# Optimization experiments

Measured on AMD Instinct MI355X. Metric: run time of the kernel, lower is better.

Reference implementation:

```python
import jax, jax.numpy as jnp
import numpy as np
from jax import lax

BN_EPS = 1e-5


def conv3x3(x, w):
    # x: [B,C,H,W], w: [O,I,3,3] -> [B,O,H,W], stride 1, SAME padding, no bias
    return lax.conv_general_dilated(x, w, (1, 1), 'SAME',
                                    dimension_numbers=('NCHW', 'OIHW', 'NCHW'))


def batchnorm_eval(x, gamma, beta, mean, var):
    inv = gamma / jnp.sqrt(var + BN_EPS)
    return x * inv[None, :, None, None] + (beta - mean * inv)[None, :, None, None]


def avg_pool3(x):
    # AvgPool2d(3, stride=1, padding=1) with count_include_pad=True -> sum/9
    s = lax.reduce_window(x, 0.0, lax.add, (1, 1, 3, 3), (1, 1, 1, 1), 'SAME')
    return s / 9.0


def max_pool3(x):
    return lax.reduce_window(x, -jnp.inf, lax.max, (1, 1, 3, 3), (1, 1, 1, 1), 'SAME')


def setup_inputs() -> dict:
    key = jax.random.key(0)
    ks = jax.random.split(key, 20)
    B, C, H, W = 8, 256, 48, 48
    sc = 0.05
    inp = {
        'ftr': jax.random.normal(ks[0], (B, C, H, W), jnp.float32),
        'wq': jax.random.normal(ks[1], (C, C, 1, 1), jnp.float32) * sc,
        'bq': jax.random.normal(ks[2], (C,), jnp.float32) * sc,
        'wk': jax.random.normal(ks[3], (C, C, 1, 1), jnp.float32) * sc,
        'bk': jax.random.normal(ks[4], (C,), jnp.float32) * sc,
        'wv': jax.random.normal(ks[5], (C, C, 1, 1), jnp.float32) * sc,
        'bv': jax.random.normal(ks[6], (C,), jnp.float32) * sc,
        'delta': jnp.array([0.1], jnp.float32),
        'w_rbc': jax.random.normal(ks[7], (C, C, 3, 3), jnp.float32) * sc,
        'g1': jnp.ones((C,), jnp.float32),
        'b1': jnp.zeros((C,), jnp.float32),
        'm1': jnp.zeros((C,), jnp.float32),
        'v1': jnp.ones((C,), jnp.float32),
        'w_rbc2': jax.random.normal(ks[8], (C, 2 * C, 3, 3), jnp.float32) * sc,
        'g2': jnp.ones((C,), jnp.float32),
        'b2': jnp.zeros((C,), jnp.float32),
        'm2': jnp.zeros((C,), jnp.float32),
        'v2': jnp.ones((C,), jnp.float32),
    }
    return inp


def reference(ftr, wq, bq, wk, bk, wv, bv, delta, w_rbc, g1, b1, m1, v1,
              w_rbc2, g2, b2, m2, v2):
    B, C, H, W = ftr.shape
    P = H * W
    x = ftr.reshape(B, C, P)  # [B,C,P]
    # 1x1 convs as channel matmuls
    q = jnp.einsum('oc,bcp->bop', wq[:, :, 0, 0], x) + bq[None, :, None]
    k = jnp.einsum('oc,bcp->bop', wk[:, :, 0, 0], x) + bk[None, :, None]
    v = jnp.einsum('oc,bcp->bop', wv[:, :, 0, 0], x) + bv[None, :, None]
    # scores[b,i,j] = sum_c q[b,c,i] * k[b,c,j]; softmax over i (dim=1)
    scores = jnp.einsum('bci,bcj->bij', q, k)
    weights = jax.nn.softmax(scores, axis=1)
    G = jnp.einsum('bci,bij->bcj', v, weights).reshape(B, C, H, W)
    out = delta[0] * G + ftr
    # conv_rbc: conv3x3 -> BN(eval) -> ReLU, then sigmoid gate
    out = jax.nn.relu(batchnorm_eval(conv3x3(out, w_rbc), g1, b1, m1, v1))
    gate = jax.nn.sigmoid(out)
    ftr_avg = avg_pool3(ftr) * gate
    ftr_max = max_pool3(ftr) * gate
    cat = jnp.concatenate((ftr_max, ftr_avg), axis=1)  # [B,2C,H,W]
    out = jax.nn.relu(batchnorm_eval(conv3x3(cat, w_rbc2), g2, b2, m2, v2))
    return out
```

## Files before the change

### kernel.cpp

```cpp
#include <hip/hip_runtime.h>
#include <math.h>

#define NB   8
#define CCH  256
#define PPX  2304
#define CPb  (CCH*PPX)
#define NTOT (NB*CPb)
#define PSQ  (PPX*PPX)
#define PADIMG 2500

typedef short short8_t __attribute__((ext_vector_type(8)));
typedef float f4_t __attribute__((ext_vector_type(4)));

__device__ __forceinline__ float relu_(float x){ return x > 0.f ? x : 0.f; }

__device__ __forceinline__ unsigned short f2bf(float f) {
  unsigned int u = __builtin_bit_cast(unsigned int, f);
  u += 0x7fffu + ((u >> 16) & 1u);
  return (unsigned short)(u >> 16);
}
__device__ __forceinline__ float bf2f(unsigned short h) {
  unsigned int u = ((unsigned int)h) << 16;
  return __builtin_bit_cast(float, u);
}
__device__ __forceinline__ unsigned int pack2(float a, float b) {
  return (unsigned int)f2bf(a) | ((unsigned int)f2bf(b) << 16);
}

__device__ __forceinline__ void gll16(const void* g, void* l) {
  __builtin_amdgcn_global_load_lds(
      (const __attribute__((address_space(1))) unsigned int*)g,
      (__attribute__((address_space(3))) unsigned int*)l, 16, 0, 0);
}

__global__ __launch_bounds__(256) void castw(
    const float* __restrict__ w, unsigned short* __restrict__ o, int n)
{
  const int i = blockIdx.x * 256 + threadIdx.x;
  if (i < n) o[i] = f2bf(w[i]);
}

__global__ __launch_bounds__(256) void repack_w(
    const float* __restrict__ w, unsigned short* __restrict__ wr, int Cin)
{
  const int idx = blockIdx.x * 256 + threadIdx.x;
  const int total = 9 * 256 * Cin;
  if (idx >= total) return;
  const int c = idx % Cin;
  const int rest = idx / Cin;
  const int o = rest % 256;
  const int tap = rest / 256;
  wr[idx] = f2bf(w[((size_t)o * Cin + c) * 9 + tap]);
}

__global__ __launch_bounds__(256) void transpose_cast(
    const float* __restrict__ ftr, unsigned short* __restrict__ xt)
{
  const int p0 = blockIdx.x * 64, c0 = blockIdx.y * 64, b = blockIdx.z;
  const int t = threadIdx.x;
  __shared__ unsigned short T[64][72];
  #pragma unroll
  for (int pass = 0; pass < 4; pass++) {
    const int cr = pass * 16 + (t >> 4);
    const int pc = (t & 15) * 4;
    float4 v = *(const float4*)&ftr[((size_t)(b * 256 + c0 + cr)) * PPX + p0 + pc];
    T[pc + 0][cr] = f2bf(v.x); T[pc + 1][cr] = f2bf(v.y);
    T[pc + 2][cr] = f2bf(v.z); T[pc + 3][cr] = f2bf(v.w);
  }
  __syncthreads();
  #pragma unroll
  for (int pass = 0; pass < 2; pass++) {
    const int pr = pass * 32 + (t >> 3);
    const int cc = (t & 7) * 8;
    *(uint4*)&xt[((size_t)(b * PPX + p0 + pr)) * 256 + c0 + cc] = *(const uint4*)&T[pr][cc];
  }
}

template<int EPI>
__global__ __launch_bounds__(256) void gemm_nt(
    const unsigned short* __restrict__ A, long Ab,
    const unsigned short* __restrict__ B, long Bb, int K,
    unsigned short* __restrict__ O, long Ob, int ldo,
    const float* __restrict__ bias,
    const float* __restrict__ ftr, const float* __restrict__ delta, int bstart)
{
  const int t = threadIdx.x;
  const int ln = t & 63;
  const int wid = t >> 6;
  const int wm = (wid & 1) * 64, wn = (wid >> 1) * 64;
  const int lm = ln & 15, lg = ln >> 4;
  const int m0 = blockIdx.x * 128, n0 = blockIdx.y * 128;
  const long bz = blockIdx.z;
  const unsigned short* Ap = A + bz * Ab;
  const unsigned short* Bp = B + bz * Bb;

  __shared__ __align__(16) unsigned short As[128 * 32];
  __shared__ __align__(16) unsigned short Bs[128 * 32];

  const int sR = ln >> 2, sP = ln & 3;
  const int fbase = lm * 32 + (((lg + (lm >> 2)) & 3) * 8);

  f4_t acc[4][4];
  #pragma unroll
  for (int i = 0; i < 4; i++)
    #pragma unroll
    for (int j = 0; j < 4; j++) acc[i][j] = (f4_t){0.f, 0.f, 0.f, 0.f};

  for (int k0 = 0; k0 < K; k0 += 32) {
    __syncthreads();
    #pragma unroll
    for (int i = wid; i < 8; i += 4) {
      const int R = i * 16 + sR;
      const int l = (sP - (R >> 2)) & 3;
      gll16(Ap + (size_t)(m0 + R) * K + k0 + l * 8, As + i * 512);
      gll16(Bp + (size_t)(n0 + R) * K + k0 + l * 8, Bs + i * 512);
    }
    __syncthreads();
    short8_t a[4], b[4];
    #pragma unroll
    for (int ti = 0; ti < 4; ti++)
      a[ti] = *(const short8_t*)(As + (wm + ti * 16) * 32 + fbase);
    #pragma unroll
    for (int tj = 0; tj < 4; tj++)
      b[tj] = *(const short8_t*)(Bs + (wn + tj * 16) * 32 + fbase);
    #pragma unroll
    for (int ti = 0; ti < 4; ti++)
      #pragma unroll
      for (int tj = 0; tj < 4; tj++)
        acc[ti][tj] = __builtin_amdgcn_mfma_f32_16x16x32_bf16(
            a[ti], b[tj], acc[ti][tj], 0, 0, 0);
  }

  if (EPI == 3) {
    const int b = bstart + (int)bz;
    const float d0 = delta[0];
    #pragma unroll
    for (int ti = 0; ti < 4; ti++) {
      const int mb = m0 + wm + ti * 16 + (lg << 2);
      #pragma unroll
      for (int tj = 0; tj < 4; tj++) {
        const int n = n0 + wn + tj * 16 + lm;
        const int y = n / 48, x = n - (n / 48) * 48;
        const size_t pp = (size_t)(y + 1) * 50 + (x + 1);
        float vr[4];
        #pragma unroll
        for (int r = 0; r < 4; r++)
          vr[r] = d0 * acc[ti][tj][r] + ftr[((size_t)(b * 256 + mb + r)) * PPX + n];
        uint2 o;
        o.x = pack2(vr[0], vr[1]);
        o.y = pack2(vr[2], vr[3]);
        *(uint2*)(O + ((size_t)b * PADIMG + pp) * 256 + mb) = o;
      }
    }
  } else {
    #pragma unroll
    for (int ti = 0; ti < 4; ti++) {
      const int mb = m0 + wm + ti * 16 + (lg << 2);
      #pragma unroll
      for (int tj = 0; tj < 4; tj++) {
        const int n = n0 + wn + tj * 16 + lm;
        float add0 = 0.f, add1 = 0.f, add2 = 0.f, add3 = 0.f;
        if (EPI == 1) { add0 = bias[mb]; add1 = bias[mb+1]; add2 = bias[mb+2]; add3 = bias[mb+3]; }
        if (EPI == 2) { add0 = add1 = add2 = add3 = bias[n]; }
        uint2 o;
        o.x = pack2(acc[ti][tj][0] + add0, acc[ti][tj][1] + add1);
        o.y = pack2(acc[ti][tj][2] + add2, acc[ti][tj][3] + add3);
        *(uint2*)(O + bz * Ob + (size_t)n * ldo + mb) = o;
      }
    }
  }
}

__global__ __launch_bounds__(256) void rowstats(
    unsigned short* __restrict__ St, long sstride)
{
  const int j = blockIdx.x, bb = blockIdx.y;
  unsigned short* row = St + (long)bb * sstride + (size_t)j * PPX;
  const int t = threadIdx.x;

  float v[16];
  int nv = 0;
  float m = -1e30f;
  for (int ch = t; ch < 288; ch += 256) {
    const uint4 d = *(const uint4*)(row + ch * 8);
    const unsigned int* dp = (const unsigned int*)&d;
    #pragma unroll
    for (int q = 0; q < 4; q++) {
      v[nv]     = bf2f((unsigned short)(dp[q] & 0xffffu));
      v[nv + 1] = bf2f((unsigned short)(dp[q] >> 16));
      m = fmaxf(m, fmaxf(v[nv], v[nv + 1]));
      nv += 2;
    }
  }
  __shared__ float red[256];
  red[t] = m; __syncthreads();
  for (int s = 128; s > 0; s >>= 1) {
    if (t < s) red[t] = fmaxf(red[t], red[t + s]);
    __syncthreads();
  }
  m = red[0]; __syncthreads();
  float sum = 0.f;
  for (int u = 0; u < nv; u++) { v[u] = expf(v[u] - m); sum += v[u]; }
  red[t] = sum; __syncthreads();
  for (int s = 128; s > 0; s >>= 1) {
    if (t < s) red[t] += red[t + s];
    __syncthreads();
  }
  const float inv = 1.f / red[0];
  int u = 0;
  for (int ch = t; ch < 288; ch += 256) {
    unsigned int res[4];
    #pragma unroll
    for (int q = 0; q < 4; q++) {
      res[q] = pack2(v[u] * inv, v[u + 1] * inv);
      u += 2;
    }
    *(uint4*)(row + ch * 8) = *(const uint4*)res;
  }
}

template<bool OUT_BF16>
__global__ __launch_bounds__(128) void conv_mfma(
    const unsigned short* __restrict__ act_p, int Cin,
    const unsigned short* __restrict__ wr,
    const float* __restrict__ gamma, const float* __restrict__ beta,
    const float* __restrict__ mean,  const float* __restrict__ var,
    void* __restrict__ outv)
{
  const int t  = threadIdx.x;
  const int wv = t >> 6;
  const int ln = t & 63;
  const int lm = ln & 15;
  const int lg = ln >> 4;

  const int bx = blockIdx.x;
  const int bb = bx / 18;
  const int p0 = (bx % 18) * 128;
  const int m0 = blockIdx.y * 64;

  __shared__ __align__(16) unsigned short Bs[240 * 32];
  __shared__ __align__(16) unsigned short As[9 * 64 * 32];

  const int qbase = p0 + 2 * (p0 / 48);
  int qoff[4];
  #pragma unroll
  for (int tj = 0; tj < 4; tj++) {
    const int p = p0 + wv * 64 + tj * 16 + lm;
    qoff[tj] = (p - p0) + 2 * (p / 48 - p0 / 48) + 51;
  }

  const int sR = ln >> 2, sP = ln & 3;
  const int abase = lm * 32 + (((lg + (lm >> 2)) & 3) * 8);

  f4_t acc[4][4];
  #pragma unroll
  for (int i = 0; i < 4; i++)
    #pragma unroll
    for (int j = 0; j < 4; j++) acc[i][j] = (f4_t){0.f, 0.f, 0.f, 0.f};

  for (int c0 = 0; c0 < Cin; c0 += 32) {
    __syncthreads();
    const unsigned short* gb = act_p + ((size_t)bb * PADIMG) * Cin + c0;
    for (int i = wv; i < 15; i += 2) {
      const int R = i * 16 + sR;
      int Rg = qbase + R;
      if (Rg > PADIMG - 1) Rg = PADIMG - 1;
      const int l = (sP - (R >> 2)) & 3;
      gll16(gb + (size_t)Rg * Cin + l * 8, Bs + i * 512);
    }
    for (int i = wv; i < 36; i += 2) {
      const int R = i * 16 + sR;
      const int tap = R >> 6, mr = R & 63;
      const int l = (sP - (R >> 2)) & 3;
      gll16(wr + ((size_t)(tap * 256 + m0 + mr)) * Cin + c0 + l * 8, As + i * 512);
    }
    __syncthreads();
    #pragma unroll
    for (int ky = 0; ky < 3; ky++) {
      #pragma unroll
      for (int kx = 0; kx < 3; kx++) {
        const int off = (ky - 1) * 50 + (kx - 1);
        const int tap = ky * 3 + kx;
        short8_t a[4], b[4];
        #pragma unroll
        for (int ti = 0; ti < 4; ti++)
          a[ti] = *(const short8_t*)(As + tap * 2048 + ti * 512 + abase);
        #pragma unroll
        for (int tj = 0; tj < 4; tj++) {
          const int R = qoff[tj] + off;
          const int slot = (lg + (R >> 2)) & 3;
          b[tj] = *(const short8_t*)(Bs + R * 32 + slot * 8);
        }
        #pragma unroll
        for (int ti = 0; ti < 4; ti++)
          #pragma unroll
          for (int tj = 0; tj < 4; tj++)
            acc[ti][tj] = __builtin_amdgcn_mfma_f32_16x16x32_bf16(
                a[ti], b[tj], acc[ti][tj], 0, 0, 0);
      }
    }
  }

  #pragma unroll
  for (int ti = 0; ti < 4; ti++) {
    const int m = m0 + ti * 16 + (lg << 2);
    float inv[4], add[4];
    #pragma unroll
    for (int r = 0; r < 4; r++) {
      inv[r] = gamma[m + r] * rsqrtf(var[m + r] + 1e-5f);
      add[r] = beta[m + r] - mean[m + r] * inv[r];
    }
    #pragma unroll
    for (int tj = 0; tj < 4; tj++) {
      const int p = p0 + wv * 64 + tj * 16 + lm;
      float vr[4];
      #pragma unroll
      for (int r = 0; r < 4; r++)
        vr[r] = relu_(acc[ti][tj][r] * inv[r] + add[r]);
      if (OUT_BF16) {
        uint2 o;
        o.x = pack2(vr[0], vr[1]);
        o.y = pack2(vr[2], vr[3]);
        *(uint2*)((unsigned short*)outv + ((size_t)(bb * PPX + p)) * 256 + m) = o;
      } else {
        #pragma unroll
        for (int r = 0; r < 4; r++)
          ((float*)outv)[((size_t)(bb * 256 + m + r)) * PPX + p] = vr[r];
      }
    }
  }
}

__global__ __launch_bounds__(256) void pool_gate_cat(
    const unsigned short* __restrict__ xt, const unsigned short* __restrict__ act1b,
    unsigned short* __restrict__ cat_p)
{
  const int idx = blockIdx.x * 256 + threadIdx.x;
  const int c = idx & 255;
  const int rest = idx >> 8;
  const int p = rest % PPX;
  const int b = rest / PPX;
  const int y = p / 48, x = p - (p / 48) * 48;
  const unsigned short* base = xt + ((size_t)b * PPX) * 256 + c;
  float s = 0.f, mxv = -1e30f;
  #pragma unroll
  for (int dy = -1; dy <= 1; dy++) {
    const int yy = y + dy;
    if (yy < 0 || yy >= 48) continue;
    #pragma unroll
    for (int dx = -1; dx <= 1; dx++) {
      const int xx = x + dx;
      if (xx < 0 || xx >= 48) continue;
      const float f = bf2f(base[(size_t)(yy * 48 + xx) * 256]);
      s += f; mxv = fmaxf(mxv, f);
    }
  }
  const float g = bf2f(act1b[(size_t)idx]);
  const float gate = 1.f / (1.f + expf(-g));
  const size_t pp = (size_t)(y + 1) * 50 + (x + 1);
  unsigned short* crow = cat_p + ((size_t)b * PADIMG + pp) * 512;
  crow[c]       = f2bf(mxv * gate);
  crow[c + 256] = f2bf(s * (1.f / 9.f) * gate);
}

extern "C" void kernel_launch(void* const* d_in, const int* in_sizes, int n_in,
                              void* d_out, int out_size, void* d_ws, size_t ws_size,
                              hipStream_t stream)
{
  const float* ftr  = (const float*)d_in[0];
  const float* wq   = (const float*)d_in[1];
  const float* bq   = (const float*)d_in[2];
  const float* wk   = (const float*)d_in[3];
  const float* bk   = (const float*)d_in[4];
  const float* wv   = (const float*)d_in[5];
  const float* bv   = (const float*)d_in[6];
  const float* delta= (const float*)d_in[7];
  const float* w1   = (const float*)d_in[8];
  const float* g1   = (const float*)d_in[9];
  const float* b1   = (const float*)d_in[10];
  const float* m1   = (const float*)d_in[11];
  const float* v1   = (const float*)d_in[12];
  const float* w2   = (const float*)d_in[13];
  const float* g2   = (const float*)d_in[14];
  const float* b2   = (const float*)d_in[15];
  const float* m2   = (const float*)d_in[16];
  const float* v2   = (const float*)d_in[17];
  float* out = (float*)d_out;

  const size_t XT = (size_t)NTOT;
  unsigned short* base = (unsigned short*)d_ws;
  unsigned short* xt   = base;
  unsigned short* qt   = xt  + XT;
  unsigned short* kt   = qt  + XT;
  unsigned short* vbuf = kt  + XT;
  unsigned short* wqb  = vbuf + XT;
  unsigned short* wkb  = wqb + 65536;
  unsigned short* wvb  = wkb + 65536;
  unsigned short* wr1  = wvb + 65536;
  unsigned short* wr2  = wr1 + (size_t)9 * 256 * 256;
  unsigned short* attn_p = wr2 + (size_t)9 * 256 * 512;
  unsigned short* act1b  = attn_p + (size_t)NB * PADIMG * 256;
  unsigned short* cat_p  = act1b + XT;
  unsigned short* St     = cat_p + (size_t)NB * PADIMG * 512;

  const size_t head_bytes = (size_t)((char*)St - (char*)base);
  const bool modeA = ws_size >= head_bytes + (size_t)NB * PSQ * 2;

  const size_t ATTN_P_SH = (size_t)NB * PADIMG * 256;
  const size_t CAT_P_SH  = (size_t)NB * PADIMG * 512;

  castw<<<dim3(256), 256, 0, stream>>>(wq, wqb, 65536);
  castw<<<dim3(256), 256, 0, stream>>>(wk, wkb, 65536);
  castw<<<dim3(256), 256, 0, stream>>>(wv, wvb, 65536);
  repack_w<<<dim3((9 * 256 * 256 + 255) / 256), 256, 0, stream>>>(w1, wr1, 256);
  repack_w<<<dim3((9 * 256 * 512 + 255) / 256), 256, 0, stream>>>(w2, wr2, 512);

  transpose_cast<<<dim3(36, 4, 8), 256, 0, stream>>>(ftr, xt);

  gemm_nt<1><<<dim3(2, 18, 8), 256, 0, stream>>>(
      wqb, 0L, xt, (long)CPb, 256, qt, (long)CPb, 256, bq, nullptr, nullptr, 0);
  gemm_nt<1><<<dim3(2, 18, 8), 256, 0, stream>>>(
      wkb, 0L, xt, (long)CPb, 256, kt, (long)CPb, 256, bk, nullptr, nullptr, 0);
  gemm_nt<2><<<dim3(18, 2, 8), 256, 0, stream>>>(
      xt, (long)CPb, wvb, 0L, 256, vbuf, (long)CPb, PPX, bv, nullptr, nullptr, 0);

  hipMemsetAsync(attn_p, 0, ATTN_P_SH * 2, stream);

  if (modeA) {
    gemm_nt<0><<<dim3(18, 18, 8), 256, 0, stream>>>(
        qt, (long)CPb, kt, (long)CPb, 256, St, (long)PSQ, PPX, nullptr, nullptr, nullptr, 0);
    rowstats<<<dim3(PPX, 8), 256, 0, stream>>>(St, (long)PSQ);
    gemm_nt<3><<<dim3(2, 18, 8), 256, 0, stream>>>(
        vbuf, (long)CPb, St, (long)PSQ, PPX, attn_p, 0L, 0, nullptr, ftr, delta, 0);
  } else {
    for (int b = 0; b < NB; b++) {
      gemm_nt<0><<<dim3(18, 18, 1), 256, 0, stream>>>(
          qt + (size_t)b * CPb, 0L, kt + (size_t)b * CPb, 0L, 256,
          St, 0L, PPX, nullptr, nullptr, nullptr, 0);
      rowstats<<<dim3(PPX, 1), 256, 0, stream>>>(St, 0L);
      gemm_nt<3><<<dim3(2, 18, 1), 256, 0, stream>>>(
          vbuf + (size_t)b * CPb, 0L, St, 0L, PPX, attn_p, 0L, 0, nullptr, ftr, delta, b);
    }
  }

  conv_mfma<true><<<dim3(144, 4), 128, 0, stream>>>(
      attn_p, 256, wr1, g1, b1, m1, v1, (void*)act1b);

  hipMemsetAsync(cat_p, 0, CAT_P_SH * 2, stream);
  pool_gate_cat<<<dim3(NTOT / 256), 256, 0, stream>>>(xt, act1b, cat_p);

  conv_mfma<false><<<dim3(144, 4), 128, 0, stream>>>(
      cat_p, 512, wr2, g2, b2, m2, v2, (void*)out);
}
```

Measured before the change: 453.7 us.

## Double-buffer GEMM and conv LDS tiles; retile conv to 288-pixel blocks

```diff
diff --git a/kernel.cpp b/kernel.cpp
--- a/kernel.cpp
+++ b/kernel.cpp
@@ -94,8 +94,8 @@
   const unsigned short* Ap = A + bz * Ab;
   const unsigned short* Bp = B + bz * Bb;
 
-  __shared__ __align__(16) unsigned short As[128 * 32];
-  __shared__ __align__(16) unsigned short Bs[128 * 32];
+  __shared__ __align__(16) unsigned short As[2][128 * 32];
+  __shared__ __align__(16) unsigned short Bs[2][128 * 32];
 
   const int sR = ln >> 2, sP = ln & 3;
   const int fbase = lm * 32 + (((lg + (lm >> 2)) & 3) * 8);
@@ -106,23 +106,37 @@
     #pragma unroll
     for (int j = 0; j < 4; j++) acc[i][j] = (f4_t){0.f, 0.f, 0.f, 0.f};
 
-  for (int k0 = 0; k0 < K; k0 += 32) {
+  const int S = K / 32;
+
+  #pragma unroll
+  for (int i = wid; i < 8; i += 4) {
+    const int R = i * 16 + sR;
+    const int l = (sP - (R >> 2)) & 3;
+    gll16(Ap + (size_t)(m0 + R) * K + l * 8, &As[0][i * 512]);
+    gll16(Bp + (size_t)(n0 + R) * K + l * 8, &Bs[0][i * 512]);
+  }
+
+  for (int s = 0; s < S; s++) {
     __syncthreads();
-    #pragma unroll
-    for (int i = wid; i < 8; i += 4) {
-      const int R = i * 16 + sR;
-      const int l = (sP - (R >> 2)) & 3;
-      gll16(Ap + (size_t)(m0 + R) * K + k0 + l * 8, As + i * 512);
-      gll16(Bp + (size_t)(n0 + R) * K + k0 + l * 8, Bs + i * 512);
-    }
-    __syncthreads();
+    if (s + 1 < S) {
+      const int kk = (s + 1) * 32;
+      #pragma unroll
+      for (int i = wid; i < 8; i += 4) {
+        const int R = i * 16 + sR;
+        const int l = (sP - (R >> 2)) & 3;
+        gll16(Ap + (size_t)(m0 + R) * K + kk + l * 8, &As[(s + 1) & 1][i * 512]);
+        gll16(Bp + (size_t)(n0 + R) * K + kk + l * 8, &Bs[(s + 1) & 1][i * 512]);
+      }
+    }
+    const unsigned short* Asb = As[s & 1];
+    const unsigned short* Bsb = Bs[s & 1];
     short8_t a[4], b[4];
     #pragma unroll
     for (int ti = 0; ti < 4; ti++)
-      a[ti] = *(const short8_t*)(As + (wm + ti * 16) * 32 + fbase);
+      a[ti] = *(const short8_t*)(Asb + (wm + ti * 16) * 32 + fbase);
     #pragma unroll
     for (int tj = 0; tj < 4; tj++)
-      b[tj] = *(const short8_t*)(Bs + (wn + tj * 16) * 32 + fbase);
+      b[tj] = *(const short8_t*)(Bsb + (wn + tj * 16) * 32 + fbase);
     #pragma unroll
     for (int ti = 0; ti < 4; ti++)
       #pragma unroll
@@ -220,7 +234,7 @@
 }
 
 template<bool OUT_BF16>
-__global__ __launch_bounds__(128) void conv_mfma(
+__global__ __launch_bounds__(256) void conv_mfma(
     const unsigned short* __restrict__ act_p, int Cin,
     const unsigned short* __restrict__ wr,
     const float* __restrict__ gamma, const float* __restrict__ beta,
@@ -228,82 +242,86 @@
     void* __restrict__ outv)
 {
   const int t  = threadIdx.x;
-  const int wv = t >> 6;
+  const int wid = t >> 6;
   const int ln = t & 63;
   const int lm = ln & 15;
   const int lg = ln >> 4;
+  const int wm  = wid & 1;
+  const int wpx = wid >> 1;
 
   const int bx = blockIdx.x;
-  const int bb = bx / 18;
-  const int p0 = (bx % 18) * 128;
+  const int bb = bx >> 3;
+  const int p0 = (bx & 7) * 288;
   const int m0 = blockIdx.y * 64;
 
-  __shared__ __align__(16) unsigned short Bs[240 * 32];
-  __shared__ __align__(16) unsigned short As[9 * 64 * 32];
+  __shared__ __align__(16) unsigned short Bs[2][400 * 32];
 
   const int qbase = p0 + 2 * (p0 / 48);
-  int qoff[4];
-  #pragma unroll
-  for (int tj = 0; tj < 4; tj++) {
-    const int p = p0 + wv * 64 + tj * 16 + lm;
-    qoff[tj] = (p - p0) + 2 * (p / 48 - p0 / 48) + 51;
-  }
-
+  int qoff[9];
+  #pragma unroll
+  for (int tj = 0; tj < 9; tj++) {
+    const int dp = wpx * 144 + tj * 16 + lm;
+    qoff[tj] = dp + 2 * (dp / 48) + 51;
+  }
   const int sR = ln >> 2, sP = ln & 3;
-  const int abase = lm * 32 + (((lg + (lm >> 2)) & 3) * 8);
-
-  f4_t acc[4][4];
-  #pragma unroll
-  for (int i = 0; i < 4; i++)
-    #pragma unroll
-    for (int j = 0; j < 4; j++) acc[i][j] = (f4_t){0.f, 0.f, 0.f, 0.f};
-
-  for (int c0 = 0; c0 < Cin; c0 += 32) {
+
+  f4_t acc[2][9];
+  #pragma unroll
+  for (int i = 0; i < 2; i++)
+    #pragma unroll
+    for (int j = 0; j < 9; j++) acc[i][j] = (f4_t){0.f, 0.f, 0.f, 0.f};
+
+  const unsigned short* gb = act_p + (size_t)bb * PADIMG * Cin;
+
+  for (int i = wid; i < 25; i += 4) {
+    const int R = i * 16 + sR;
+    const int l = (sP - (R >> 2)) & 3;
+    gll16(gb + (size_t)(qbase + R) * Cin + l * 8, &Bs[0][i * 512]);
+  }
+
+  const int S = Cin / 32;
+  for (int s = 0; s < S; s++) {
     __syncthreads();
-    const unsigned short* gb = act_p + ((size_t)bb * PADIMG) * Cin + c0;
-    for (int i = wv; i < 15; i += 2) {
-      const int R = i * 16 + sR;
-      int Rg = qbase + R;
-      if (Rg > PADIMG - 1) Rg = PADIMG - 1;
-      const int l = (sP - (R >> 2)) & 3;
-      gll16(gb + (size_t)Rg * Cin + l * 8, Bs + i * 512);
-    }
-    for (int i = wv; i < 36; i += 2) {
-      const int R = i * 16 + sR;
-      const int tap = R >> 6, mr = R & 63;
-      const int l = (sP - (R >> 2)) & 3;
-      gll16(wr + ((size_t)(tap * 256 + m0 + mr)) * Cin + c0 + l * 8, As + i * 512);
-    }
-    __syncthreads();
+    const int c0 = s * 32;
+    short8_t a[2][9];
+    #pragma unroll
+    for (int tap = 0; tap < 9; tap++)
+      #pragma unroll
+      for (int ti = 0; ti < 2; ti++)
+        a[ti][tap] = *(const short8_t*)(wr +
+            ((size_t)(tap * 256 + m0 + wm * 32 + ti * 16 + lm)) * Cin + c0 + lg * 8);
+    if (s + 1 < S) {
+      const int cn = c0 + 32;
+      for (int i = wid; i < 25; i += 4) {
+        const int R = i * 16 + sR;
+        const int l = (sP - (R >> 2)) & 3;
+        gll16(gb + (size_t)(qbase + R) * Cin + cn + l * 8, &Bs[(s + 1) & 1][i * 512]);
+      }
+    }
+    const unsigned short* Bsb = Bs[s & 1];
     #pragma unroll
     for (int ky = 0; ky < 3; ky++) {
       #pragma unroll
       for (int kx = 0; kx < 3; kx++) {
         const int off = (ky - 1) * 50 + (kx - 1);
         const int tap = ky * 3 + kx;
-        short8_t a[4], b[4];
         #pragma unroll
-        for (int ti = 0; ti < 4; ti++)
-          a[ti] = *(const short8_t*)(As + tap * 2048 + ti * 512 + abase);
-        #pragma unroll
-        for (int tj = 0; tj < 4; tj++) {
+        for (int tj = 0; tj < 9; tj++) {
           const int R = qoff[tj] + off;
           const int slot = (lg + (R >> 2)) & 3;
-          b[tj] = *(const short8_t*)(Bs + R * 32 + slot * 8);
+          const short8_t bfr = *(const short8_t*)(Bsb + R * 32 + slot * 8);
+          acc[0][tj] = __builtin_amdgcn_mfma_f32_16x16x32_bf16(
+              a[0][tap], bfr, acc[0][tj], 0, 0, 0);
+          acc[1][tj] = __builtin_amdgcn_mfma_f32_16x16x32_bf16(
+              a[1][tap], bfr, acc[1][tj], 0, 0, 0);
         }
-        #pragma unroll
-        for (int ti = 0; ti < 4; ti++)
-          #pragma unroll
-          for (int tj = 0; tj < 4; tj++)
-            acc[ti][tj] = __builtin_amdgcn_mfma_f32_16x16x32_bf16(
-                a[ti], b[tj], acc[ti][tj], 0, 0, 0);
-      }
-    }
-  }
-
-  #pragma unroll
-  for (int ti = 0; ti < 4; ti++) {
-    const int m = m0 + ti * 16 + (lg << 2);
+      }
+    }
+  }
+
+  #pragma unroll
+  for (int ti = 0; ti < 2; ti++) {
+    const int m = m0 + wm * 32 + ti * 16 + (lg << 2);
     float inv[4], add[4];
     #pragma unroll
     for (int r = 0; r < 4; r++) {
@@ -311,8 +329,8 @@
       add[r] = beta[m + r] - mean[m + r] * inv[r];
     }
     #pragma unroll
-    for (int tj = 0; tj < 4; tj++) {
-      const int p = p0 + wv * 64 + tj * 16 + lm;
+    for (int tj = 0; tj < 9; tj++) {
+      const int p = p0 + wpx * 144 + tj * 16 + lm;
       float vr[4];
       #pragma unroll
       for (int r = 0; r < 4; r++)
@@ -443,12 +461,12 @@
     }
   }
 
-  conv_mfma<true><<<dim3(144, 4), 128, 0, stream>>>(
+  conv_mfma<true><<<dim3(64, 4), 256, 0, stream>>>(
       attn_p, 256, wr1, g1, b1, m1, v1, (void*)act1b);
 
   hipMemsetAsync(cat_p, 0, CAT_P_SH * 2, stream);
   pool_gate_cat<<<dim3(NTOT / 256), 256, 0, stream>>>(xt, act1b, cat_p);
 
-  conv_mfma<false><<<dim3(144, 4), 128, 0, stream>>>(
+  conv_mfma<false><<<dim3(64, 4), 256, 0, stream>>>(
       cat_p, 512, wr2, g2, b2, m2, v2, (void*)out);
 }
```

Result: slower. 499.3 us (+10.1%).
